# Performance work log

Hardware: AMD Instinct MI355X
Metric: run time of the kernel (lower is better)

## Reference

```python
import jax, jax.numpy as jnp
import numpy as np

B, H, LB, PW, TC = 4096, 64, 32, 16, 1
WL = LB + PW  # window_length = look_back + prediction


def setup_inputs() -> dict:
    key = jax.random.key(0)
    ks = jax.random.split(key, 9)
    bnd = 1.0 / np.sqrt(H)  # torch Linear default init bound
    bnd_h = 1.0 / np.sqrt(H)
    return {
        "x": jax.random.normal(ks[0], (B, LB, TC), jnp.float32),
        "F_w": jax.random.uniform(ks[1], (WL, H, H), jnp.float32, -bnd, bnd),
        "F_b": jax.random.uniform(ks[2], (WL, H), jnp.float32, -bnd, bnd),
        "H_w": jax.random.uniform(ks[3], (WL, TC, H), jnp.float32, -bnd_h, bnd_h),
        "H_b": jax.random.uniform(ks[4], (WL, TC), jnp.float32, -bnd_h, bnd_h),
        "initial_state": jax.random.normal(ks[5], (H,), jnp.float32),
        "initial_covariance": 0.1 * jax.random.normal(ks[6], (H, H), jnp.float32),
        "Q": 0.1 * jax.random.normal(ks[7], (H, H), jnp.float32),
        "R": jnp.eye(TC, dtype=jnp.float32) + 0.1 * jax.random.normal(ks[8], (TC, TC), jnp.float32),
    }


def _kalman_forward(x, F_w, F_b, H_w, H_b, s0, P0, Q, R):
    nb = x.shape[0]
    hs = jnp.broadcast_to(s0, (nb, H))          # (B,H)
    P = jnp.broadcast_to(P0, (nb, H, H))        # (B,H,H)
    ys = jnp.moveaxis(x[:, :LB, :TC], 0, 1)     # (LB,B,TC) per-step observations

    @jax.checkpoint
    def kf_step(carry, inp):
        hs, P = carry
        Fw, Fb, Hw, Hb, y = inp
        hs_pred = hs @ Fw.T + Fb                                        # (B,H)
        P_pred = jnp.einsum('ij,bjk,lk->bil', Fw, P, Fw) + Q            # F P F^T + Q
        resid = y - (hs_pred @ Hw.T + Hb)                               # (B,TC)
        S = jnp.einsum('ij,bjk,lk->bil', Hw, P_pred, Hw) + R            # (B,TC,TC)
        K = jnp.einsum('bij,kj->bik', P_pred, Hw) @ jnp.linalg.inv(S)   # (B,H,TC)
        hs_new = hs_pred + jnp.einsum('bij,bj->bi', K, resid)
        P_new = P_pred - jnp.einsum('bit,tj,bjk->bik', K, Hw, P_pred)   # (I-KH)P_pred
        return (hs_new, P_new), None

    (hs, _), _ = jax.lax.scan(
        kf_step, (hs, P), (F_w[:LB], F_b[:LB], H_w[:LB], H_b[:LB], ys))

    def pred_step(hs, inp):
        Fw, Fb, Hw, Hb = inp
        hs = hs @ Fw.T + Fb
        return hs, hs @ Hw.T + Hb

    _, ems = jax.lax.scan(
        pred_step, hs, (F_w[LB:], F_b[LB:], H_w[LB:], H_b[LB:]))  # (PW,B,TC)
    # torch.cat(preds, dim=1).unsqueeze(-1) -> (B, PW*TC, 1)
    return jnp.moveaxis(ems, 0, 1).reshape(nb, PW * TC)[..., None]


def reference(x, F_w, F_b, H_w, H_b, initial_state, initial_covariance, Q, R):
    return _kalman_forward(x, F_w, F_b, H_w, H_b, initial_state, initial_covariance, Q, R)
```

## Files before the change

kernel.cpp:

```cpp
#include <hip/hip_runtime.h>


constexpr int Hn  = 64;
constexpr int LBn = 32;
constexpr int PWn = 16;
constexpr int NC  = 33;

constexpr int WOFF_W = 0;
constexpr int WOFF_U = NC * Hn;
constexpr int WOFF_E = WOFF_U + PWn * Hn;
constexpr int WOFF_K = WOFF_E + PWn;

typedef float  f32x4 __attribute__((ext_vector_type(4)));
typedef _Float16 f16x4 __attribute__((ext_vector_type(4)));
typedef _Float16 f16x8 __attribute__((ext_vector_type(8)));

#define MFMA16(a, b, c) __builtin_amdgcn_mfma_f32_16x16x16f16((a), (b), (c), 0, 0, 0)

__global__ __launch_bounds__(512) void kalmanA(
    const float* __restrict__ Fw, const float* __restrict__ Fb,
    const float* __restrict__ Hw, const float* __restrict__ Hb,
    const float* __restrict__ s0, const float* __restrict__ P0,
    const float* __restrict__ Qg, const float* __restrict__ Rg,
    float* __restrict__ ws) {
  const int tid  = threadIdx.x;
  const int lane = tid & 63;
  const int w    = tid >> 6;

  if (blockIdx.x == 1) {
    for (int pi = 0; pi < 2; ++pi) {
      const int p = pi ? (15 - w) : w;
      const int q = LBn + p;
      float r = Hw[q * Hn + lane];
      float eacc = 0.f;
      for (int s = 0; s <= p; ++s) {
        const int m = q - s;
        eacc += r * Fb[m * Hn + lane];
        const float* Fm = Fw + (size_t)m * Hn * Hn;
        float rn = 0.f;
        for (int j = 0; j < Hn; ++j)
          rn += __shfl(r, j, 64) * Fm[j * Hn + lane];
        r = rn;
      }
      #pragma unroll
      for (int o = 32; o >= 1; o >>= 1) eacc += __shfl_xor(eacc, o, 64);
      ws[WOFF_U + p * Hn + lane] = r;
      if (lane == 0) ws[WOFF_E + p] = eacc + Hb[q];
    }
    return;
  }

  __shared__ _Float16 Ffrag[16][65][8];
  __shared__ float    Tfrag[16][64][4];
  __shared__ float    Pfrag[16][64][5];
  __shared__ float    nred[2][64], mred[4][64], hv[64];

  const float R0 = Rg[0];
  const int l15 = lane & 15, g = lane >> 4;
  const int ti = w >> 1, half = w & 1;
  const int lp0 = 16 * (l15 >> 2) + 4 * g;
  const int rg  = l15 & 3;
  const int sr = tid >> 3, sc0 = (tid & 7) * 8;
  const int fi = (sr >> 4) * 4 + (sc0 >> 4);
  const int L0 = (sr & 15) + 16 * ((sc0 >> 2) & 3);
  float* kws = ws + WOFF_K;

  float qf[2][4];
  #pragma unroll
  for (int s2 = 0; s2 < 2; ++s2)
    #pragma unroll
    for (int reg = 0; reg < 4; ++reg)
      qf[s2][reg] = Qg[(16 * ti + 4 * g + reg) * 64 + l15 + 16 * (2 * half + s2)];

  #pragma unroll
  for (int u = 0; u < 8; ++u) {
    const int cc = sc0 + u;
    Pfrag[(sr >> 4) * 4 + (cc >> 4)][16 * ((sr & 15) >> 2) + (cc & 15)][sr & 3] =
        P0[sr * 64 + cc];
  }
  f32x4 fpa = *(const f32x4*)(Fw + sr * 64 + sc0);
  f32x4 fpb = *(const f32x4*)(Fw + sr * 64 + sc0 + 4);
  __syncthreads();

  float kv = 0.f, mr = 0.f;
  for (int t = 0; t < LBn; ++t) {
    if (t > 0) {
      const float n = nred[0][lane] + nred[1][lane];
      mr = mred[0][lane] + mred[1][lane] + mred[2][lane] + mred[3][lane];
      float s = hv[lane] * n;
      #pragma unroll
      for (int o = 32; o >= 1; o >>= 1) s += __shfl_xor(s, o, 64);
      kv = n / (s + R0);
      if (w == 0) kws[(t - 1) * 64 + lane] = kv;
    } else { kv = 0.f; mr = 0.f; }

    const float kr = __shfl(kv, l15 + 16 * ti, 64);
    f16x4 Ah[4], Al[4];
    #pragma unroll
    for (int kc = 0; kc < 4; ++kc) {
      #pragma unroll
      for (int j = 0; j < 4; ++j) {
        const float mcol = __shfl(mr, 16 * kc + 4 * g + j, 64);
        const float pv = Pfrag[ti * 4 + kc][lp0 + j][rg] - kr * mcol;
        const _Float16 hi_ = (_Float16)pv;
        Ah[kc][j] = hi_;
        Al[kc][j] = (_Float16)((pv - (float)hi_) * 2048.0f);
      }
    }
    {
      f16x8 pa, pb;
      #pragma unroll
      for (int u = 0; u < 4; ++u) {
        const _Float16 ha = (_Float16)fpa[u];
        pa[u] = ha; pa[4 + u] = (_Float16)((fpa[u] - (float)ha) * 2048.0f);
        const _Float16 hb = (_Float16)fpb[u];
        pb[u] = hb; pb[4 + u] = (_Float16)((fpb[u] - (float)hb) * 2048.0f);
      }
      *(f16x8*)&Ffrag[fi][L0][0]      = pa;
      *(f16x8*)&Ffrag[fi][L0 + 16][0] = pb;
    }
    __syncthreads();

    if (t + 1 < LBn) {
      fpa = *(const f32x4*)(Fw + (size_t)(t + 1) * 4096 + sr * 64 + sc0);
      fpb = *(const f32x4*)(Fw + (size_t)(t + 1) * 4096 + sr * 64 + sc0 + 4);
    }
    if (w == 0) hv[lane] = Hw[t * 64 + lane];
    #pragma unroll
    for (int s2 = 0; s2 < 2; ++s2) {
      const int tj = 2 * half + s2;
      f32x4 accm = {0.f, 0.f, 0.f, 0.f}, accc = {0.f, 0.f, 0.f, 0.f};
      #pragma unroll
      for (int kc = 0; kc < 4; ++kc) {
        const f16x8 bv = *(const f16x8*)&Ffrag[tj * 4 + kc][lane][0];
        const f16x4 bh = __builtin_shufflevector(bv, bv, 0, 1, 2, 3);
        const f16x4 bl = __builtin_shufflevector(bv, bv, 4, 5, 6, 7);
        accm = MFMA16(Ah[kc], bh, accm);
        accc = MFMA16(Ah[kc], bl, accc);
        accc = MFMA16(Al[kc], bh, accc);
      }
      const f32x4 outv = accm + accc * (1.0f / 2048.0f);
      *(f32x4*)&Tfrag[ti * 4 + tj][lane][0] = outv;
    }
    __syncthreads();

    f16x4 FAh[4], FAl[4];
    #pragma unroll
    for (int kc = 0; kc < 4; ++kc) {
      const f16x8 av = *(const f16x8*)&Ffrag[ti * 4 + kc][lane][0];
      FAh[kc] = __builtin_shufflevector(av, av, 0, 1, 2, 3);
      FAl[kc] = __builtin_shufflevector(av, av, 4, 5, 6, 7);
    }
    f32x4 pout[2];
    #pragma unroll
    for (int s2 = 0; s2 < 2; ++s2) {
      const int tj = 2 * half + s2;
      f32x4 accm = {0.f, 0.f, 0.f, 0.f}, accc = {0.f, 0.f, 0.f, 0.f};
      #pragma unroll
      for (int kc = 0; kc < 4; ++kc) {
        const f32x4 tv = *(const f32x4*)&Tfrag[kc * 4 + tj][lane][0];
        f16x4 th, tl;
        #pragma unroll
        for (int j = 0; j < 4; ++j) {
          const _Float16 hi_ = (_Float16)tv[j];
          th[j] = hi_;
          tl[j] = (_Float16)((tv[j] - (float)hi_) * 2048.0f);
        }
        accm = MFMA16(FAh[kc], th, accm);
        accc = MFMA16(FAh[kc], tl, accc);
        accc = MFMA16(FAl[kc], th, accc);
      }
      pout[s2] = accm + accc * (1.0f / 2048.0f);
      #pragma unroll
      for (int reg = 0; reg < 4; ++reg) {
        pout[s2][reg] += qf[s2][reg];
        Pfrag[ti * 4 + tj][lane][reg] = pout[s2][reg];
      }
    }
    {
      const float hc0 = hv[l15 + 16 * (2 * half)];
      const float hc1 = hv[l15 + 16 * (2 * half + 1)];
      float np[4];
      #pragma unroll
      for (int reg = 0; reg < 4; ++reg)
        np[reg] = pout[0][reg] * hc0 + pout[1][reg] * hc1;
      #pragma unroll
      for (int m = 1; m <= 8; m <<= 1)
        #pragma unroll
        for (int reg = 0; reg < 4; ++reg)
          np[reg] += __shfl_xor(np[reg], m, 64);
      if (l15 == 0) {
        #pragma unroll
        for (int reg = 0; reg < 4; ++reg)
          nred[half][16 * ti + 4 * g + reg] = np[reg];
      }
      float hr[4];
      #pragma unroll
      for (int reg = 0; reg < 4; ++reg) hr[reg] = hv[16 * ti + 4 * g + reg];
      float mp0 = 0.f, mp1 = 0.f;
      #pragma unroll
      for (int reg = 0; reg < 4; ++reg) {
        mp0 += pout[0][reg] * hr[reg];
        mp1 += pout[1][reg] * hr[reg];
      }
      mp0 += __shfl_xor(mp0, 16, 64); mp0 += __shfl_xor(mp0, 32, 64);
      mp1 += __shfl_xor(mp1, 16, 64); mp1 += __shfl_xor(mp1, 32, 64);
      if (g == 0) {
        mred[ti][l15 + 16 * (2 * half)]     = mp0;
        mred[ti][l15 + 16 * (2 * half + 1)] = mp1;
      }
    }
    __syncthreads();
  }

  {
    const float n = nred[0][lane] + nred[1][lane];
    float s = hv[lane] * n;
    #pragma unroll
    for (int o = 32; o >= 1; o >>= 1) s += __shfl_xor(s, o, 64);
    if (w == 0) kws[31 * 64 + lane] = n / (s + R0);
  }
}

__global__ __launch_bounds__(64) void kalmanC(
    const float* __restrict__ Fw, const float* __restrict__ Fb,
    const float* __restrict__ Hw, const float* __restrict__ Hb,
    const float* __restrict__ s0, float* __restrict__ ws) {
  const int c = blockIdx.x;
  const int lane = threadIdx.x;
  const float* kws = ws + WOFF_K;
  if (c == 32) {
    ws[WOFF_W + 32 * 64 + lane] = kws[31 * 64 + lane];
    return;
  }
  __shared__ float vbuf[64];
  float v; int t0;
  if (c == 0) { v = s0[lane]; t0 = 0; }
  else        { v = kws[(c - 1) * 64 + lane]; t0 = c; }

  f32x4 fn[16];
  {
    const float* Fr = Fw + (size_t)t0 * 4096 + lane * 64;
    #pragma unroll
    for (int jc = 0; jc < 16; ++jc) fn[jc] = *(const f32x4*)(Fr + jc * 4);
  }
  for (int t = t0; t < 32; ++t) {
    vbuf[lane] = v;
    __syncthreads();
    f32x4 fc[16];
    #pragma unroll
    for (int jc = 0; jc < 16; ++jc) fc[jc] = fn[jc];
    if (t + 1 < 32) {
      const float* Fr = Fw + (size_t)(t + 1) * 4096 + lane * 64;
      #pragma unroll
      for (int jc = 0; jc < 16; ++jc) fn[jc] = *(const f32x4*)(Fr + jc * 4);
    }
    float vp = (c == 0) ? Fb[t * 64 + lane] : 0.f;
    #pragma unroll
    for (int jc = 0; jc < 16; ++jc) {
      const f32x4 vb = *(const f32x4*)&vbuf[jc * 4];
      vp += fc[jc].x * vb.x + fc[jc].y * vb.y + fc[jc].z * vb.z + fc[jc].w * vb.w;
    }
    float hvp = Hw[t * 64 + lane] * vp;
    #pragma unroll
    for (int o = 32; o >= 1; o >>= 1) hvp += __shfl_xor(hvp, o, 64);
    if (c == 0) hvp += Hb[t];
    v = vp - kws[t * 64 + lane] * hvp;
    __syncthreads();
  }
  ws[WOFF_W + c * 64 + lane] = v;
}

__global__ __launch_bounds__(256) void kalmanB(
    const float* __restrict__ x, const float* __restrict__ ws,
    float* __restrict__ out) {
  __shared__ float Zl[PWn][NC + 1];
  __shared__ float xs[256 * NC];
  const int tid = threadIdx.x;
  const int b0  = blockIdx.x * 256;

  for (int idx = tid; idx < PWn * NC; idx += 256) {
    const int p = idx / NC, c = idx % NC;
    const float* Up = ws + WOFF_U + p * Hn;
    const float* Wc = ws + WOFF_W + c * Hn;
    float acc = 0.f;
    for (int i = 0; i < Hn; ++i) acc += Up[i] * Wc[i];
    if (c == 0) acc += ws[WOFF_E + p];
    Zl[p][c] = acc;
  }
  const float4* xv = (const float4*)(x + (size_t)b0 * LBn);
  #pragma unroll
  for (int r = 0; r < 8; ++r) {
    const int fi = tid + 256 * r;
    const float4 v = xv[fi];
    const int b  = fi >> 3;
    const int t0 = (fi & 7) * 4;
    float* d = &xs[b * NC + t0];
    d[0] = v.x; d[1] = v.y; d[2] = v.z; d[3] = v.w;
  }
  __syncthreads();

  const int b = tid;
  float acc[PWn];
  #pragma unroll
  for (int p = 0; p < PWn; ++p) acc[p] = Zl[p][0];
  for (int t = 0; t < LBn; ++t) {
    const float xval = xs[b * NC + t];
    #pragma unroll
    for (int p = 0; p < PWn; ++p) acc[p] += Zl[p][1 + t] * xval;
  }
  float4* op = (float4*)(out + (size_t)(b0 + b) * PWn);
  op[0] = make_float4(acc[0], acc[1], acc[2], acc[3]);
  op[1] = make_float4(acc[4], acc[5], acc[6], acc[7]);
  op[2] = make_float4(acc[8], acc[9], acc[10], acc[11]);
  op[3] = make_float4(acc[12], acc[13], acc[14], acc[15]);
}

extern "C" void kernel_launch(void* const* d_in, const int* in_sizes, int n_in,
                              void* d_out, int out_size, void* d_ws, size_t ws_size,
                              hipStream_t stream) {
  const float* x  = (const float*)d_in[0];
  const float* Fw = (const float*)d_in[1];
  const float* Fb = (const float*)d_in[2];
  const float* Hw = (const float*)d_in[3];
  const float* Hb = (const float*)d_in[4];
  const float* s0 = (const float*)d_in[5];
  const float* P0 = (const float*)d_in[6];
  const float* Q  = (const float*)d_in[7];
  const float* R  = (const float*)d_in[8];
  float* ws  = (float*)d_ws;
  float* out = (float*)d_out;

  kalmanA<<<2, 512, 0, stream>>>(Fw, Fb, Hw, Hb, s0, P0, Q, R, ws);
  kalmanC<<<33, 64, 0, stream>>>(Fw, Fb, Hw, Hb, s0, ws);
  kalmanB<<<16, 256, 0, stream>>>(x, ws, out);
}
```

Before: 152.8 us.

## Fuse three Kalman kernels into one with tagged flag-based inter-block handoff

Merges the covariance recursion, state-propagation chains, and batch output kernels into a single persistent launch. Blocks exchange Kalman gains and intermediate vectors through tagged 64-bit atomic words in workspace, so each gain step can be consumed as soon as it is published. The covariance loop also drops one barrier per step by storing the intermediate product in split fp16 form and staging the next F after the first barrier, and reductions use DPP. The risks are spin-waiting that relies on all 15 blocks being co-resident, plus an added memset launch.

```diff
diff --git a/kernel.cpp b/kernel.cpp
--- a/kernel.cpp
+++ b/kernel.cpp
@@ -1,324 +1,365 @@
 #include <hip/hip_runtime.h>
 
 
-constexpr int Hn  = 64;
-constexpr int LBn = 32;
-constexpr int PWn = 16;
-constexpr int NC  = 33;
-
-constexpr int WOFF_W = 0;
-constexpr int WOFF_U = NC * Hn;
-constexpr int WOFF_E = WOFF_U + PWn * Hn;
-constexpr int WOFF_K = WOFF_E + PWn;
-
-typedef float  f32x4 __attribute__((ext_vector_type(4)));
+constexpr int KP_OFF = 0;
+constexpr int WP_OFF = 2048;
+constexpr int UP_OFF = 4160;
+constexpr int EP_OFF = 5184;
+constexpr int WS_U64 = 5200;
+
+typedef float    f32x4 __attribute__((ext_vector_type(4)));
 typedef _Float16 f16x4 __attribute__((ext_vector_type(4)));
 typedef _Float16 f16x8 __attribute__((ext_vector_type(8)));
 
 #define MFMA16(a, b, c) __builtin_amdgcn_mfma_f32_16x16x16f16((a), (b), (c), 0, 0, 0)
 
-__global__ __launch_bounds__(512) void kalmanA(
+template <int CTRL>
+__device__ __forceinline__ float dpp_add(float x) {
+  int v = __builtin_amdgcn_update_dpp(0, __builtin_bit_cast(int, x), CTRL, 0xf, 0xf, true);
+  return x + __builtin_bit_cast(float, v);
+}
+__device__ __forceinline__ float sum16(float x) {
+  x = dpp_add<0xB1>(x);
+  x = dpp_add<0x4E>(x);
+  x = dpp_add<0x141>(x);
+  x = dpp_add<0x140>(x);
+  return x;
+}
+__device__ __forceinline__ float sum64(float x) {
+  x = sum16(x);
+  x += __shfl_xor(x, 16, 64);
+  x += __shfl_xor(x, 32, 64);
+  return x;
+}
+
+__device__ __forceinline__ float spin_read(const unsigned long long* p, unsigned tag) {
+  unsigned long long v = 0;
+  for (int it = 0; it < (1 << 22); ++it) {
+    v = __hip_atomic_load(p, __ATOMIC_RELAXED, __HIP_MEMORY_SCOPE_AGENT);
+    if ((unsigned)(v >> 32) == tag) break;
+  }
+  union { unsigned u; float f; } cv; cv.u = (unsigned)v;
+  return cv.f;
+}
+__device__ __forceinline__ void pub_write(unsigned long long* p, unsigned tag, float x) {
+  union { float f; unsigned u; } cv; cv.f = x;
+  __hip_atomic_store(p, ((unsigned long long)tag << 32) | cv.u,
+                     __ATOMIC_RELAXED, __HIP_MEMORY_SCOPE_AGENT);
+}
+
+__global__ __launch_bounds__(512) void kalman_fused(
     const float* __restrict__ Fw, const float* __restrict__ Fb,
     const float* __restrict__ Hw, const float* __restrict__ Hb,
     const float* __restrict__ s0, const float* __restrict__ P0,
     const float* __restrict__ Qg, const float* __restrict__ Rg,
-    float* __restrict__ ws) {
+    const float* __restrict__ x, float* __restrict__ out,
+    unsigned long long* __restrict__ ws) {
+  __shared__ __align__(16) char smem[55040];
   const int tid  = threadIdx.x;
   const int lane = tid & 63;
   const int w    = tid >> 6;
-
-  if (blockIdx.x == 1) {
+  const int blk  = blockIdx.x;
+  unsigned long long* kp = ws + KP_OFF;
+  unsigned long long* wp = ws + WP_OFF;
+  unsigned long long* up = ws + UP_OFF;
+  unsigned long long* ep = ws + EP_OFF;
+
+  if (blk == 0) {
+    _Float16* FF  = (_Float16*)smem;
+    _Float16* TF  = (_Float16*)(smem + 16640);
+    float*    PF  = (float*)(smem + 33024);
+    float*    nred = (float*)(smem + 53504);
+    float*    mred = (float*)(smem + 54016);
+
+    const int l15 = lane & 15, g = lane >> 4;
+    const int ti = w >> 1, half = w & 1;
+    const int lp0 = 16 * (l15 >> 2) + 4 * g;
+    const int rg  = l15 & 3;
+    const int sr = tid >> 3, sc0 = (tid & 7) * 8;
+    const int fi = (sr >> 4) * 4 + (sc0 >> 4);
+    const int L0 = (sr & 15) + 16 * ((sc0 >> 2) & 3);
+    const float R0 = Rg[0];
+
+    auto FFp = [&](int f, int l) { return FF + (f * 65 + l) * 8; };
+    auto TFp = [&](int f, int l) { return TF + (f * 64 + l) * 8; };
+    auto PFi = [&](int f, int l, int r) { return (f * 64 + l) * 5 + r; };
+
+    auto stageF = [&](f32x4 a, f32x4 b) {
+      f16x8 pa, pb;
+      #pragma unroll
+      for (int u = 0; u < 4; ++u) {
+        const _Float16 ha = (_Float16)a[u];
+        pa[u] = ha; pa[4 + u] = (_Float16)((a[u] - (float)ha) * 2048.0f);
+        const _Float16 hb = (_Float16)b[u];
+        pb[u] = hb; pb[4 + u] = (_Float16)((b[u] - (float)hb) * 2048.0f);
+      }
+      *(f16x8*)FFp(fi, L0)      = pa;
+      *(f16x8*)FFp(fi, L0 + 16) = pb;
+    };
+
+    float qf0[4], qf1[4];
+    #pragma unroll
+    for (int reg = 0; reg < 4; ++reg) {
+      qf0[reg] = Qg[(16 * ti + 4 * g + reg) * 64 + 16 * (2 * half) + l15];
+      qf1[reg] = Qg[(16 * ti + 4 * g + reg) * 64 + 16 * (2 * half + 1) + l15];
+    }
+    #pragma unroll
+    for (int u = 0; u < 8; ++u) {
+      const int cc = sc0 + u;
+      PF[PFi((sr >> 4) * 4 + (cc >> 4), 16 * ((sr & 15) >> 2) + (cc & 15), sr & 3)] =
+          P0[sr * 64 + cc];
+    }
+    f32x4 fpa = *(const f32x4*)(Fw + sr * 64 + sc0);
+    f32x4 fpb = *(const f32x4*)(Fw + sr * 64 + sc0 + 4);
+    stageF(fpa, fpb);
+    float hcur = Hw[lane], hprev = 0.f, hnext = 0.f;
+    __syncthreads();
+
+    for (int t = 0; t < 32; ++t) {
+      float kv = 0.f, mr = 0.f;
+      if (t > 0) {
+        const float n = nred[lane] + nred[64 + lane];
+        mr = mred[lane] + mred[64 + lane] + mred[128 + lane] + mred[192 + lane];
+        const float s = sum64(hprev * n);
+        kv = n / (s + R0);
+        if (w == 0) pub_write(&kp[(t - 1) * 64 + lane], (unsigned)t, kv);
+      }
+      if (t + 1 < 32) {
+        fpa = *(const f32x4*)(Fw + (size_t)(t + 1) * 4096 + sr * 64 + sc0);
+        fpb = *(const f32x4*)(Fw + (size_t)(t + 1) * 4096 + sr * 64 + sc0 + 4);
+        hnext = Hw[(t + 1) * 64 + lane];
+      }
+      const float kr = __shfl(kv, l15 + 16 * ti, 64);
+      f16x4 Ah[4], Al[4];
+      #pragma unroll
+      for (int kc = 0; kc < 4; ++kc) {
+        #pragma unroll
+        for (int j = 0; j < 4; ++j) {
+          const float mcol = __shfl(mr, 16 * kc + 4 * g + j, 64);
+          const float pv = PF[PFi(ti * 4 + kc, lp0 + j, rg)] - kr * mcol;
+          const _Float16 hi_ = (_Float16)pv;
+          Ah[kc][j] = hi_;
+          Al[kc][j] = (_Float16)((pv - (float)hi_) * 2048.0f);
+        }
+      }
+      f16x4 FAh[4], FAl[4];
+      #pragma unroll
+      for (int kc = 0; kc < 4; ++kc) {
+        const f16x8 av = *(const f16x8*)FFp(ti * 4 + kc, lane);
+        FAh[kc] = __builtin_shufflevector(av, av, 0, 1, 2, 3);
+        FAl[kc] = __builtin_shufflevector(av, av, 4, 5, 6, 7);
+      }
+      #pragma unroll
+      for (int s2 = 0; s2 < 2; ++s2) {
+        const int tj = 2 * half + s2;
+        f32x4 am = {0.f, 0.f, 0.f, 0.f}, a1 = {0.f, 0.f, 0.f, 0.f}, a2 = {0.f, 0.f, 0.f, 0.f};
+        #pragma unroll
+        for (int kc = 0; kc < 4; ++kc) {
+          const f16x8 bv = *(const f16x8*)FFp(tj * 4 + kc, lane);
+          const f16x4 bh = __builtin_shufflevector(bv, bv, 0, 1, 2, 3);
+          const f16x4 bl = __builtin_shufflevector(bv, bv, 4, 5, 6, 7);
+          am = MFMA16(Ah[kc], bh, am);
+          a1 = MFMA16(Ah[kc], bl, a1);
+          a2 = MFMA16(Al[kc], bh, a2);
+        }
+        const f32x4 outv = am + (a1 + a2) * (1.0f / 2048.0f);
+        f16x8 tv;
+        #pragma unroll
+        for (int j = 0; j < 4; ++j) {
+          const _Float16 hi_ = (_Float16)outv[j];
+          tv[j] = hi_;
+          tv[4 + j] = (_Float16)((outv[j] - (float)hi_) * 2048.0f);
+        }
+        *(f16x8*)TFp(ti * 4 + tj, lane) = tv;
+      }
+      __syncthreads();
+
+      if (t + 1 < 32) stageF(fpa, fpb);
+      f32x4 pout[2];
+      #pragma unroll
+      for (int s2 = 0; s2 < 2; ++s2) {
+        const int tj = 2 * half + s2;
+        f32x4 am = {0.f, 0.f, 0.f, 0.f}, a1 = {0.f, 0.f, 0.f, 0.f}, a2 = {0.f, 0.f, 0.f, 0.f};
+        #pragma unroll
+        for (int kc = 0; kc < 4; ++kc) {
+          const f16x8 bv = *(const f16x8*)TFp(kc * 4 + tj, lane);
+          const f16x4 bh = __builtin_shufflevector(bv, bv, 0, 1, 2, 3);
+          const f16x4 bl = __builtin_shufflevector(bv, bv, 4, 5, 6, 7);
+          am = MFMA16(FAh[kc], bh, am);
+          a1 = MFMA16(FAh[kc], bl, a1);
+          a2 = MFMA16(FAl[kc], bh, a2);
+        }
+        pout[s2] = am + (a1 + a2) * (1.0f / 2048.0f);
+        #pragma unroll
+        for (int reg = 0; reg < 4; ++reg) {
+          pout[s2][reg] += (s2 ? qf1[reg] : qf0[reg]);
+          PF[PFi(ti * 4 + tj, lane, reg)] = pout[s2][reg];
+        }
+      }
+      const float hcA = __shfl(hcur, 16 * (2 * half) + l15, 64);
+      const float hcB = __shfl(hcur, 16 * (2 * half + 1) + l15, 64);
+      float hr[4];
+      #pragma unroll
+      for (int reg = 0; reg < 4; ++reg) hr[reg] = __shfl(hcur, 16 * ti + 4 * g + reg, 64);
+      #pragma unroll
+      for (int reg = 0; reg < 4; ++reg) {
+        float np = pout[0][reg] * hcA + pout[1][reg] * hcB;
+        np = sum16(np);
+        if (l15 == 0) nred[half * 64 + 16 * ti + 4 * g + reg] = np;
+      }
+      float mp0 = 0.f, mp1 = 0.f;
+      #pragma unroll
+      for (int reg = 0; reg < 4; ++reg) {
+        mp0 += pout[0][reg] * hr[reg];
+        mp1 += pout[1][reg] * hr[reg];
+      }
+      mp0 += __shfl_xor(mp0, 16, 64); mp0 += __shfl_xor(mp0, 32, 64);
+      mp1 += __shfl_xor(mp1, 16, 64); mp1 += __shfl_xor(mp1, 32, 64);
+      if (g == 0) {
+        mred[ti * 64 + 16 * (2 * half) + l15]     = mp0;
+        mred[ti * 64 + 16 * (2 * half + 1) + l15] = mp1;
+      }
+      __syncthreads();
+      hprev = hcur; hcur = hnext;
+    }
+    {
+      const float n = nred[lane] + nred[64 + lane];
+      const float s = sum64(hprev * n);
+      if (w == 0) pub_write(&kp[31 * 64 + lane], 32u, n / (s + R0));
+    }
+    return;
+  }
+
+  if (blk == 1) {
     for (int pi = 0; pi < 2; ++pi) {
       const int p = pi ? (15 - w) : w;
-      const int q = LBn + p;
-      float r = Hw[q * Hn + lane];
+      const int q = 32 + p;
+      float r = Hw[q * 64 + lane];
       float eacc = 0.f;
       for (int s = 0; s <= p; ++s) {
         const int m = q - s;
-        eacc += r * Fb[m * Hn + lane];
-        const float* Fm = Fw + (size_t)m * Hn * Hn;
-        float rn = 0.f;
-        for (int j = 0; j < Hn; ++j)
-          rn += __shfl(r, j, 64) * Fm[j * Hn + lane];
-        r = rn;
-      }
-      #pragma unroll
-      for (int o = 32; o >= 1; o >>= 1) eacc += __shfl_xor(eacc, o, 64);
-      ws[WOFF_U + p * Hn + lane] = r;
-      if (lane == 0) ws[WOFF_E + p] = eacc + Hb[q];
+        eacc += r * Fb[m * 64 + lane];
+        const float* Fm = Fw + (size_t)m * 4096;
+        float r0 = 0.f, r1 = 0.f, r2 = 0.f, r3 = 0.f;
+        for (int j = 0; j < 64; j += 4) {
+          r0 += __shfl(r, j,     64) * Fm[j * 64 + lane];
+          r1 += __shfl(r, j + 1, 64) * Fm[(j + 1) * 64 + lane];
+          r2 += __shfl(r, j + 2, 64) * Fm[(j + 2) * 64 + lane];
+          r3 += __shfl(r, j + 3, 64) * Fm[(j + 3) * 64 + lane];
+        }
+        r = (r0 + r1) + (r2 + r3);
+      }
+      eacc = sum64(eacc);
+      pub_write(&up[p * 64 + lane], 1u, r);
+      if (lane == 0) pub_write(&ep[p], 1u, eacc + Hb[q]);
     }
     return;
   }
 
-  __shared__ _Float16 Ffrag[16][65][8];
-  __shared__ float    Tfrag[16][64][4];
-  __shared__ float    Pfrag[16][64][5];
-  __shared__ float    nred[2][64], mred[4][64], hv[64];
-
-  const float R0 = Rg[0];
-  const int l15 = lane & 15, g = lane >> 4;
-  const int ti = w >> 1, half = w & 1;
-  const int lp0 = 16 * (l15 >> 2) + 4 * g;
-  const int rg  = l15 & 3;
-  const int sr = tid >> 3, sc0 = (tid & 7) * 8;
-  const int fi = (sr >> 4) * 4 + (sc0 >> 4);
-  const int L0 = (sr & 15) + 16 * ((sc0 >> 2) & 3);
-  float* kws = ws + WOFF_K;
-
-  float qf[2][4];
-  #pragma unroll
-  for (int s2 = 0; s2 < 2; ++s2)
-    #pragma unroll
-    for (int reg = 0; reg < 4; ++reg)
-      qf[s2][reg] = Qg[(16 * ti + 4 * g + reg) * 64 + l15 + 16 * (2 * half + s2)];
-
-  #pragma unroll
-  for (int u = 0; u < 8; ++u) {
-    const int cc = sc0 + u;
-    Pfrag[(sr >> 4) * 4 + (cc >> 4)][16 * ((sr & 15) >> 2) + (cc & 15)][sr & 3] =
-        P0[sr * 64 + cc];
-  }
-  f32x4 fpa = *(const f32x4*)(Fw + sr * 64 + sc0);
-  f32x4 fpb = *(const f32x4*)(Fw + sr * 64 + sc0 + 4);
-  __syncthreads();
-
-  float kv = 0.f, mr = 0.f;
-  for (int t = 0; t < LBn; ++t) {
-    if (t > 0) {
-      const float n = nred[0][lane] + nred[1][lane];
-      mr = mred[0][lane] + mred[1][lane] + mred[2][lane] + mred[3][lane];
-      float s = hv[lane] * n;
-      #pragma unroll
-      for (int o = 32; o >= 1; o >>= 1) s += __shfl_xor(s, o, 64);
-      kv = n / (s + R0);
-      if (w == 0) kws[(t - 1) * 64 + lane] = kv;
-    } else { kv = 0.f; mr = 0.f; }
-
-    const float kr = __shfl(kv, l15 + 16 * ti, 64);
-    f16x4 Ah[4], Al[4];
-    #pragma unroll
-    for (int kc = 0; kc < 4; ++kc) {
-      #pragma unroll
-      for (int j = 0; j < 4; ++j) {
-        const float mcol = __shfl(mr, 16 * kc + 4 * g + j, 64);
-        const float pv = Pfrag[ti * 4 + kc][lp0 + j][rg] - kr * mcol;
-        const _Float16 hi_ = (_Float16)pv;
-        Ah[kc][j] = hi_;
-        Al[kc][j] = (_Float16)((pv - (float)hi_) * 2048.0f);
-      }
-    }
+  if (blk < 7) {
+    float* vb = (float*)smem + w * 64;
+    const int c = (blk - 2) * 8 + w;
+    if (c > 32) return;
+    if (c == 32) {
+      pub_write(&wp[32 * 64 + lane], 1u, spin_read(&kp[31 * 64 + lane], 32u));
+      return;
+    }
+    const int t0 = (c == 0) ? 0 : c;
+    float v = (c == 0) ? s0[lane] : spin_read(&kp[(c - 1) * 64 + lane], (unsigned)c);
+    f32x4 fn[16];
     {
-      f16x8 pa, pb;
-      #pragma unroll
-      for (int u = 0; u < 4; ++u) {
-        const _Float16 ha = (_Float16)fpa[u];
-        pa[u] = ha; pa[4 + u] = (_Float16)((fpa[u] - (float)ha) * 2048.0f);
-        const _Float16 hb = (_Float16)fpb[u];
-        pb[u] = hb; pb[4 + u] = (_Float16)((fpb[u] - (float)hb) * 2048.0f);
-      }
-      *(f16x8*)&Ffrag[fi][L0][0]      = pa;
-      *(f16x8*)&Ffrag[fi][L0 + 16][0] = pb;
-    }
+      const float* Fr = Fw + (size_t)t0 * 4096 + lane * 64;
+      #pragma unroll
+      for (int jc = 0; jc < 16; ++jc) fn[jc] = *(const f32x4*)(Fr + jc * 4);
+    }
+    float hn  = Hw[t0 * 64 + lane];
+    float fbn = (c == 0) ? Fb[t0 * 64 + lane] : 0.f;
+    for (int t = t0; t < 32; ++t) {
+      vb[lane] = v;
+      f32x4 fc[16];
+      #pragma unroll
+      for (int jc = 0; jc < 16; ++jc) fc[jc] = fn[jc];
+      const float ht = hn, fbt = fbn;
+      if (t + 1 < 32) {
+        const float* Fr = Fw + (size_t)(t + 1) * 4096 + lane * 64;
+        #pragma unroll
+        for (int jc = 0; jc < 16; ++jc) fn[jc] = *(const f32x4*)(Fr + jc * 4);
+        hn = Hw[(t + 1) * 64 + lane];
+        if (c == 0) fbn = Fb[(t + 1) * 64 + lane];
+      }
+      float a0 = fbt, a1 = 0.f, a2 = 0.f, a3 = 0.f;
+      #pragma unroll
+      for (int jc = 0; jc < 16; ++jc) {
+        const f32x4 vv = *(const f32x4*)(vb + jc * 4);
+        a0 += fc[jc].x * vv.x; a1 += fc[jc].y * vv.y;
+        a2 += fc[jc].z * vv.z; a3 += fc[jc].w * vv.w;
+      }
+      const float vp = (a0 + a1) + (a2 + a3);
+      float hv = sum64(ht * vp);
+      if (c == 0) hv += Hb[t];
+      const float kt = spin_read(&kp[t * 64 + lane], (unsigned)(t + 1));
+      v = vp - kt * hv;
+    }
+    pub_write(&wp[c * 64 + lane], 1u, v);
+    return;
+  }
+
+  {
+    float* Ul = (float*)smem;
+    float* Wl = (float*)(smem + 4352);
+    float* Zl = (float*)(smem + 13328);
+    float* El = (float*)(smem + 15504);
+    for (int idx = tid; idx < 1024; idx += 512)
+      Ul[(idx >> 6) * 68 + (idx & 63)] = spin_read(&up[idx], 1u);
+    for (int idx = tid; idx < 2112; idx += 512)
+      Wl[(idx >> 6) * 68 + (idx & 63)] = spin_read(&wp[idx], 1u);
+    if (tid < 16) El[tid] = spin_read(&ep[tid], 1u);
     __syncthreads();
-
-    if (t + 1 < LBn) {
-      fpa = *(const f32x4*)(Fw + (size_t)(t + 1) * 4096 + sr * 64 + sc0);
-      fpb = *(const f32x4*)(Fw + (size_t)(t + 1) * 4096 + sr * 64 + sc0 + 4);
-    }
-    if (w == 0) hv[lane] = Hw[t * 64 + lane];
-    #pragma unroll
-    for (int s2 = 0; s2 < 2; ++s2) {
-      const int tj = 2 * half + s2;
-      f32x4 accm = {0.f, 0.f, 0.f, 0.f}, accc = {0.f, 0.f, 0.f, 0.f};
-      #pragma unroll
-      for (int kc = 0; kc < 4; ++kc) {
-        const f16x8 bv = *(const f16x8*)&Ffrag[tj * 4 + kc][lane][0];
-        const f16x4 bh = __builtin_shufflevector(bv, bv, 0, 1, 2, 3);
-        const f16x4 bl = __builtin_shufflevector(bv, bv, 4, 5, 6, 7);
-        accm = MFMA16(Ah[kc], bh, accm);
-        accc = MFMA16(Ah[kc], bl, accc);
-        accc = MFMA16(Al[kc], bh, accc);
-      }
-      const f32x4 outv = accm + accc * (1.0f / 2048.0f);
-      *(f32x4*)&Tfrag[ti * 4 + tj][lane][0] = outv;
-    }
+    for (int idx = tid; idx < 528; idx += 512) {
+      const int p = idx / 33, cc = idx - p * 33;
+      const float* Up = Ul + p * 68;
+      const float* Wc = Wl + cc * 68;
+      float a0 = 0.f, a1 = 0.f, a2 = 0.f, a3 = 0.f;
+      #pragma unroll 4
+      for (int i = 0; i < 64; i += 4) {
+        a0 += Up[i] * Wc[i];     a1 += Up[i + 1] * Wc[i + 1];
+        a2 += Up[i + 2] * Wc[i + 2]; a3 += Up[i + 3] * Wc[i + 3];
+      }
+      float z = (a0 + a1) + (a2 + a3);
+      if (cc == 0) z += El[p];
+      Zl[p * 34 + cc] = z;
+    }
+    const int b = (blk - 7) * 512 + tid;
+    f32x4 xr[8];
+    const f32x4* xp = (const f32x4*)(x + (size_t)b * 32);
+    #pragma unroll
+    for (int u = 0; u < 8; ++u) xr[u] = xp[u];
     __syncthreads();
-
-    f16x4 FAh[4], FAl[4];
-    #pragma unroll
-    for (int kc = 0; kc < 4; ++kc) {
-      const f16x8 av = *(const f16x8*)&Ffrag[ti * 4 + kc][lane][0];
-      FAh[kc] = __builtin_shufflevector(av, av, 0, 1, 2, 3);
-      FAl[kc] = __builtin_shufflevector(av, av, 4, 5, 6, 7);
-    }
-    f32x4 pout[2];
-    #pragma unroll
-    for (int s2 = 0; s2 < 2; ++s2) {
-      const int tj = 2 * half + s2;
-      f32x4 accm = {0.f, 0.f, 0.f, 0.f}, accc = {0.f, 0.f, 0.f, 0.f};
-      #pragma unroll
-      for (int kc = 0; kc < 4; ++kc) {
-        const f32x4 tv = *(const f32x4*)&Tfrag[kc * 4 + tj][lane][0];
-        f16x4 th, tl;
-        #pragma unroll
-        for (int j = 0; j < 4; ++j) {
-          const _Float16 hi_ = (_Float16)tv[j];
-          th[j] = hi_;
-          tl[j] = (_Float16)((tv[j] - (float)hi_) * 2048.0f);
-        }
-        accm = MFMA16(FAh[kc], th, accm);
-        accc = MFMA16(FAh[kc], tl, accc);
-        accc = MFMA16(FAl[kc], th, accc);
-      }
-      pout[s2] = accm + accc * (1.0f / 2048.0f);
-      #pragma unroll
-      for (int reg = 0; reg < 4; ++reg) {
-        pout[s2][reg] += qf[s2][reg];
-        Pfrag[ti * 4 + tj][lane][reg] = pout[s2][reg];
-      }
-    }
-    {
-      const float hc0 = hv[l15 + 16 * (2 * half)];
-      const float hc1 = hv[l15 + 16 * (2 * half + 1)];
-      float np[4];
-      #pragma unroll
-      for (int reg = 0; reg < 4; ++reg)
-        np[reg] = pout[0][reg] * hc0 + pout[1][reg] * hc1;
-      #pragma unroll
-      for (int m = 1; m <= 8; m <<= 1)
-        #pragma unroll
-        for (int reg = 0; reg < 4; ++reg)
-          np[reg] += __shfl_xor(np[reg], m, 64);
-      if (l15 == 0) {
-        #pragma unroll
-        for (int reg = 0; reg < 4; ++reg)
-          nred[half][16 * ti + 4 * g + reg] = np[reg];
-      }
-      float hr[4];
-      #pragma unroll
-      for (int reg = 0; reg < 4; ++reg) hr[reg] = hv[16 * ti + 4 * g + reg];
-      float mp0 = 0.f, mp1 = 0.f;
-      #pragma unroll
-      for (int reg = 0; reg < 4; ++reg) {
-        mp0 += pout[0][reg] * hr[reg];
-        mp1 += pout[1][reg] * hr[reg];
-      }
-      mp0 += __shfl_xor(mp0, 16, 64); mp0 += __shfl_xor(mp0, 32, 64);
-      mp1 += __shfl_xor(mp1, 16, 64); mp1 += __shfl_xor(mp1, 32, 64);
-      if (g == 0) {
-        mred[ti][l15 + 16 * (2 * half)]     = mp0;
-        mred[ti][l15 + 16 * (2 * half + 1)] = mp1;
-      }
-    }
-    __syncthreads();
-  }
-
-  {
-    const float n = nred[0][lane] + nred[1][lane];
-    float s = hv[lane] * n;
-    #pragma unroll
-    for (int o = 32; o >= 1; o >>= 1) s += __shfl_xor(s, o, 64);
-    if (w == 0) kws[31 * 64 + lane] = n / (s + R0);
-  }
-}
-
-__global__ __launch_bounds__(64) void kalmanC(
-    const float* __restrict__ Fw, const float* __restrict__ Fb,
-    const float* __restrict__ Hw, const float* __restrict__ Hb,
-    const float* __restrict__ s0, float* __restrict__ ws) {
-  const int c = blockIdx.x;
-  const int lane = threadIdx.x;
-  const float* kws = ws + WOFF_K;
-  if (c == 32) {
-    ws[WOFF_W + 32 * 64 + lane] = kws[31 * 64 + lane];
-    return;
-  }
-  __shared__ float vbuf[64];
-  float v; int t0;
-  if (c == 0) { v = s0[lane]; t0 = 0; }
-  else        { v = kws[(c - 1) * 64 + lane]; t0 = c; }
-
-  f32x4 fn[16];
-  {
-    const float* Fr = Fw + (size_t)t0 * 4096 + lane * 64;
-    #pragma unroll
-    for (int jc = 0; jc < 16; ++jc) fn[jc] = *(const f32x4*)(Fr + jc * 4);
-  }
-  for (int t = t0; t < 32; ++t) {
-    vbuf[lane] = v;
-    __syncthreads();
-    f32x4 fc[16];
-    #pragma unroll
-    for (int jc = 0; jc < 16; ++jc) fc[jc] = fn[jc];
-    if (t + 1 < 32) {
-      const float* Fr = Fw + (size_t)(t + 1) * 4096 + lane * 64;
-      #pragma unroll
-      for (int jc = 0; jc < 16; ++jc) fn[jc] = *(const f32x4*)(Fr + jc * 4);
-    }
-    float vp = (c == 0) ? Fb[t * 64 + lane] : 0.f;
-    #pragma unroll
-    for (int jc = 0; jc < 16; ++jc) {
-      const f32x4 vb = *(const f32x4*)&vbuf[jc * 4];
-      vp += fc[jc].x * vb.x + fc[jc].y * vb.y + fc[jc].z * vb.z + fc[jc].w * vb.w;
-    }
-    float hvp = Hw[t * 64 + lane] * vp;
-    #pragma unroll
-    for (int o = 32; o >= 1; o >>= 1) hvp += __shfl_xor(hvp, o, 64);
-    if (c == 0) hvp += Hb[t];
-    v = vp - kws[t * 64 + lane] * hvp;
-    __syncthreads();
-  }
-  ws[WOFF_W + c * 64 + lane] = v;
-}
-
-__global__ __launch_bounds__(256) void kalmanB(
-    const float* __restrict__ x, const float* __restrict__ ws,
-    float* __restrict__ out) {
-  __shared__ float Zl[PWn][NC + 1];
-  __shared__ float xs[256 * NC];
-  const int tid = threadIdx.x;
-  const int b0  = blockIdx.x * 256;
-
-  for (int idx = tid; idx < PWn * NC; idx += 256) {
-    const int p = idx / NC, c = idx % NC;
-    const float* Up = ws + WOFF_U + p * Hn;
-    const float* Wc = ws + WOFF_W + c * Hn;
-    float acc = 0.f;
-    for (int i = 0; i < Hn; ++i) acc += Up[i] * Wc[i];
-    if (c == 0) acc += ws[WOFF_E + p];
-    Zl[p][c] = acc;
-  }
-  const float4* xv = (const float4*)(x + (size_t)b0 * LBn);
-  #pragma unroll
-  for (int r = 0; r < 8; ++r) {
-    const int fi = tid + 256 * r;
-    const float4 v = xv[fi];
-    const int b  = fi >> 3;
-    const int t0 = (fi & 7) * 4;
-    float* d = &xs[b * NC + t0];
-    d[0] = v.x; d[1] = v.y; d[2] = v.z; d[3] = v.w;
-  }
-  __syncthreads();
-
-  const int b = tid;
-  float acc[PWn];
-  #pragma unroll
-  for (int p = 0; p < PWn; ++p) acc[p] = Zl[p][0];
-  for (int t = 0; t < LBn; ++t) {
-    const float xval = xs[b * NC + t];
-    #pragma unroll
-    for (int p = 0; p < PWn; ++p) acc[p] += Zl[p][1 + t] * xval;
-  }
-  float4* op = (float4*)(out + (size_t)(b0 + b) * PWn);
-  op[0] = make_float4(acc[0], acc[1], acc[2], acc[3]);
-  op[1] = make_float4(acc[4], acc[5], acc[6], acc[7]);
-  op[2] = make_float4(acc[8], acc[9], acc[10], acc[11]);
-  op[3] = make_float4(acc[12], acc[13], acc[14], acc[15]);
+    float acc[16];
+    #pragma unroll
+    for (int p = 0; p < 16; ++p) acc[p] = Zl[p * 34];
+    #pragma unroll
+    for (int u = 0; u < 8; ++u) {
+      #pragma unroll
+      for (int e = 0; e < 4; ++e) {
+        const float xval = xr[u][e];
+        const int t = u * 4 + e;
+        #pragma unroll
+        for (int p = 0; p < 16; ++p) acc[p] += Zl[p * 34 + 1 + t] * xval;
+      }
+    }
+    float4* op = (float4*)(out + (size_t)b * 16);
+    op[0] = make_float4(acc[0], acc[1], acc[2], acc[3]);
+    op[1] = make_float4(acc[4], acc[5], acc[6], acc[7]);
+    op[2] = make_float4(acc[8], acc[9], acc[10], acc[11]);
+    op[3] = make_float4(acc[12], acc[13], acc[14], acc[15]);
+  }
 }
 
 extern "C" void kernel_launch(void* const* d_in, const int* in_sizes, int n_in,
                               void* d_out, int out_size, void* d_ws, size_t ws_size,
                               hipStream_t stream) {
+  (void)in_sizes; (void)n_in; (void)out_size; (void)ws_size;
   const float* x  = (const float*)d_in[0];
   const float* Fw = (const float*)d_in[1];
   const float* Fb = (const float*)d_in[2];
@@ -328,10 +369,9 @@
   const float* P0 = (const float*)d_in[6];
   const float* Q  = (const float*)d_in[7];
   const float* R  = (const float*)d_in[8];
-  float* ws  = (float*)d_ws;
   float* out = (float*)d_out;
-
-  kalmanA<<<2, 512, 0, stream>>>(Fw, Fb, Hw, Hb, s0, P0, Q, R, ws);
-  kalmanC<<<33, 64, 0, stream>>>(Fw, Fb, Hw, Hb, s0, ws);
-  kalmanB<<<16, 256, 0, stream>>>(x, ws, out);
-}
+  unsigned long long* ws = (unsigned long long*)d_ws;
+
+  hipMemsetAsync(d_ws, 0, WS_U64 * sizeof(unsigned long long), stream);
+  kalman_fused<<<15, 512, 0, stream>>>(Fw, Fb, Hw, Hb, s0, P0, Q, R, x, out, ws);
+}
```

Measured after the change: 127.7 us. -16.4%, faster.
